# Kernel tuning notes

Hardware: AMD Instinct MI355X
Metric: run time of the kernel (lower is better)

## Reference

```python
import jax, jax.numpy as jnp
import numpy as np
from jax import lax

B, CIN, COUT, H, W = 16, 320, 320, 64, 64
R, NUM_LORAS, LORA_STRIDE, SCALE, K = 4, 50, 4, 1.0, 3


def setup_inputs() -> dict:
    key = jax.random.key(0)
    k1, k2, k3, k4, k5, k6 = jax.random.split(key, 6)
    x = jax.random.normal(k1, (B, CIN, H, W), dtype=jnp.float32)
    lora_id = jax.random.randint(k2, (B,), 0, NUM_LORAS * LORA_STRIDE, dtype=jnp.int64)
    conv_w = jax.random.normal(k3, (COUT, CIN, K, K), dtype=jnp.float32) * (1.0 / np.sqrt(CIN * K * K))
    conv_b = jax.random.normal(k4, (COUT,), dtype=jnp.float32) * 0.01
    # stacked LoRA banks: down [L, r, Cin, 3, 3], up [L, Cout, r] (1x1 conv squeezed)
    down_w = jax.random.normal(k5, (NUM_LORAS, R, CIN, K, K), dtype=jnp.float32) * (1.0 / R)
    up_w = jax.random.normal(k6, (NUM_LORAS, COUT, R), dtype=jnp.float32) * 0.02
    return {"x": x, "conv_w": conv_w, "conv_b": conv_b, "down_w": down_w, "up_w": up_w, "lora_id": lora_id}


def _conv3x3(x, w):
    # x: [N, C, H, W], w: [O, C, 3, 3], stride 1, padding 1
    return lax.conv_general_dilated(x, w, (1, 1), [(1, 1), (1, 1)],
                                    dimension_numbers=("NCHW", "OIHW", "NCHW"))


def reference(x, conv_w, conv_b, down_w, up_w, lora_id):
    idx = lora_id // LORA_STRIDE                      # [B]
    active = (idx >= 0).astype(x.dtype)               # [B] mask; negative -> base conv only
    safe = jnp.clip(idx, 0, NUM_LORAS - 1)
    # base conv on full batch (dropout is identity at inference)
    base = _conv3x3(x, conv_w) + conv_b[None, :, None, None]  # [B, Cout, H, W]
    # per-sample gathered down conv (3x3), vmapped over batch (MoE-style dispatch)
    wd = down_w[safe]                                 # [B, r, Cin, 3, 3]
    down = jax.vmap(lambda xi, wi: _conv3x3(xi[None], wi)[0])(x, wd)  # [B, r, H, W]
    # per-sample 1x1 up conv as einsum with gathered up weights
    up = jnp.einsum("brhw,bor->bohw", down, up_w[safe])  # [B, Cout, H, W]
    return base + SCALE * up * active[:, None, None, None]
```

## Files before the change

### kernel.cpp

```cpp
#include <hip/hip_runtime.h>

typedef unsigned short ushort_t;
typedef unsigned int   uint_t;
typedef __attribute__((ext_vector_type(8))) short  short8;
typedef __attribute__((ext_vector_type(4))) float  float4v;
typedef __attribute__((ext_vector_type(4))) uint_t uint4v;

#define B_    16
#define CIN_  320
#define COUT_ 320
#define NLORA 50
#define R_    4
#define NCH   10

#define XCHUNK (66*66*32)
#define WCHUNK (9*COUT_*32)
#define XPAD_ELEMS ((size_t)B_ * NCH * XCHUNK)
#define WEFF_OFF   (XPAD_ELEMS * 2)

__device__ __forceinline__ ushort_t bf16rne(float f) {
  uint_t u = __float_as_uint(f);
  u = (u + 0x7FFFu + ((u >> 16) & 1u)) >> 16;
  return (ushort_t)u;
}

__device__ __forceinline__ void gld16(const ushort_t* g, ushort_t* l) {
  __builtin_amdgcn_global_load_lds(
      (const __attribute__((address_space(1))) void*)g,
      (__attribute__((address_space(3))) void*)l,
      16, 0, 0);
}

__global__ __launch_bounds__(256)
void pad_convert(const float* __restrict__ x, ushort_t* __restrict__ x_pad) {
  __shared__ float t[64][65];
  const int cc  = blockIdx.x;
  const int h   = blockIdx.y;
  const int b   = blockIdx.z;
  const int tid = threadIdx.x;
  #pragma unroll
  for (int it = 0; it < 16; ++it) {
    int idx = it * 256 + tid;
    int cl = idx >> 6, wl = idx & 63;
    t[cl][wl] = x[(((size_t)(b * CIN_ + cc * 64 + cl)) * 64 + h) * 64 + wl];
  }
  __syncthreads();
  #pragma unroll
  for (int it = 0; it < 8; ++it) {
    int flat = (it * 256 + tid) * 2;
    int wl = flat >> 6, cl = flat & 63;
    uint_t u0 = bf16rne(t[cl][wl]);
    uint_t u1 = bf16rne(t[cl + 1][wl]);
    int chunk = cc * 2 + (cl >> 5);
    *(uint_t*)(x_pad + (((size_t)(b * NCH + chunk) * 66 + (h + 1)) * 66 + (wl + 1)) * 32
               + (cl & 31)) = u0 | (u1 << 16);
  }
  if (h == 0) {
    #pragma unroll
    for (int s = 0; s < 2; ++s) {
      ushort_t* base = x_pad + (size_t)(b * NCH + cc * 2 + s) * XCHUNK;
      for (int g = tid; g < 528; g += 256) {
        int r = (g >= 264) ? 1 : 0;
        int g2 = g - r * 264;
        int col = g2 >> 2, qg = g2 & 3;
        *(uint4v*)(base + ((size_t)(r * 65) * 66 + col) * 32 + qg * 8) = (uint4v)0u;
      }
      for (int g = tid; g < 512; g += 256) {
        int row = 1 + (g >> 3);
        int col = ((g >> 2) & 1) * 65;
        int qg  = g & 3;
        *(uint4v*)(base + ((size_t)row * 66 + col) * 32 + qg * 8) = (uint4v)0u;
      }
    }
  }
}

__global__ __launch_bounds__(320)
void merge_weights(const float* __restrict__ conv_w, const float* __restrict__ down_w,
                   const float* __restrict__ up_w,  const void* __restrict__ lora,
                   ushort_t* __restrict__ W_eff) {
  const int o = blockIdx.x;
  const int b = blockIdx.y;
  const int c = threadIdx.x;

  const int* p32 = (const int*)lora;
  bool odd0 = true;
  #pragma unroll
  for (int i = 1; i < 16; i += 2) odd0 = odd0 && (p32[i] == 0);
  long long raw = odd0 ? ((const long long*)lora)[b] : (long long)p32[b];
  long long idx = (raw >= 0) ? (raw >> 2) : -(((-raw) + 3) >> 2);
  float act = (idx >= 0) ? 1.0f : 0.0f;
  int l = (int)(idx < 0 ? 0 : (idx > (NLORA - 1) ? (NLORA - 1) : idx));

  float up[R_];
  #pragma unroll
  for (int r = 0; r < R_; ++r)
    up[r] = up_w[((size_t)l * COUT_ + o) * R_ + r] * act;

  const size_t wb = (size_t)(b * NCH + (c >> 5)) * 9;
  #pragma unroll
  for (int tap = 0; tap < 9; ++tap) {
    float v = conv_w[((size_t)o * CIN_ + c) * 9 + tap];
    #pragma unroll
    for (int r = 0; r < R_; ++r)
      v += up[r] * down_w[(((size_t)l * R_ + r) * CIN_ + c) * 9 + tap];
    W_eff[((wb + tap) * COUT_ + o) * 32 + (c & 31)] = bf16rne(v);
  }
}

#define XG    1360
#define XGP   1408
#define WG    1152
#define TOTG  2560
#define BUF_B (TOTG * 16)

__global__ __launch_bounds__(512, 4)
void conv_main(const ushort_t* __restrict__ x_pad, const ushort_t* __restrict__ W_eff,
               const float* __restrict__ conv_b, float* __restrict__ out) {
  __shared__ __align__(16) char smem[2 * BUF_B];

  const int tid = threadIdx.x;
  const int lin = blockIdx.x;
  const int wg  = (lin & 7) * 320 + (lin >> 3);
  const int b   = wg / 160;
  const int rem = wg - b * 160;
  const int o0  = (rem >> 4) * 32;
  const int hw  = rem & 15;
  const int h0  = (hw & 7) * 8;
  const int w0  = (hw >> 3) * 32;

  const int wv = tid >> 6;
  const int la = tid & 15;
  const int q  = (tid >> 4) & 3;

  const ushort_t* psrc[5];
  int step[5];
  #pragma unroll
  for (int r = 0; r < 5; ++r) {
    int g = r * 512 + tid;
    if (g < XGP) {
      int gx = (g < XG) ? g : (XG - 1);
      int qq = gx & 3, t = gx >> 2;
      int hh = t / 34, ww = t - hh * 34;
      psrc[r] = x_pad + (size_t)b * NCH * XCHUNK
              + (((h0 + hh) * 66 + (w0 + ww)) * 32 + qq * 8);
      step[r] = XCHUNK;
    } else {
      int gw = g - XGP;
      int qq = gw & 3, t2 = gw >> 2;
      int o = t2 & 31, tap = t2 >> 5;
      psrc[r] = W_eff + (size_t)b * NCH * WCHUNK
              + ((tap * COUT_ + o0 + o) * 32 + qq * 8);
      step[r] = WCHUNK;
    }
  }

  float4v acc[2][2];
  #pragma unroll
  for (int i = 0; i < 2; ++i)
    #pragma unroll
    for (int n = 0; n < 2; ++n) acc[i][n] = (float4v)0.0f;

  auto STAGE = [&](int sel) {
    ushort_t* bufb = (ushort_t*)(smem + sel * BUF_B);
    #pragma unroll
    for (int r = 0; r < 5; ++r) {
      gld16(psrc[r], bufb + (r * 512 + wv * 64) * 8);
      psrc[r] += step[r];
    }
  };

  STAGE(0);
  int cur = 0;
  for (int t = 0; t < NCH; ++t) {
    asm volatile("" ::: "memory");
    __builtin_amdgcn_s_barrier();
    asm volatile("" ::: "memory");
    if (t < NCH - 1) STAGE(cur ^ 1);
    __builtin_amdgcn_sched_barrier(0);
    if (t < NCH - 1) asm volatile("s_waitcnt vmcnt(5)" ::: "memory");
    else             asm volatile("s_waitcnt vmcnt(0)" ::: "memory");
    __builtin_amdgcn_sched_barrier(0);
    __builtin_amdgcn_s_barrier();
    asm volatile("" ::: "memory");

    const ushort_t* xb = (const ushort_t*)(smem + cur * BUF_B);
    const ushort_t* wb = xb + XGP * 8;
    #pragma unroll
    for (int tap = 0; tap < 9; ++tap) {
      const int kh = tap / 3, kw = tap - kh * 3;
      short8 bf0 = *(const short8*)(wb + ((tap * 32 +      la) * 4 + q) * 8);
      short8 bf1 = *(const short8*)(wb + ((tap * 32 + 16 + la) * 4 + q) * 8);
      const int hh = wv + kh;
      #pragma unroll
      for (int i = 0; i < 2; ++i) {
        short8 af = *(const short8*)(xb + ((hh * 34 + i * 16 + la + kw) * 4 + q) * 8);
        acc[i][0] = __builtin_amdgcn_mfma_f32_16x16x32_bf16(af, bf0, acc[i][0], 0, 0, 0);
        acc[i][1] = __builtin_amdgcn_mfma_f32_16x16x32_bf16(af, bf1, acc[i][1], 0, 0, 0);
      }
    }
    cur ^= 1;
  }

  __syncthreads();
  float* lc = (float*)smem;
  #pragma unroll
  for (int n = 0; n < 2; ++n) {
    const int n_loc = n * 16 + la;
    #pragma unroll
    for (int i = 0; i < 2; ++i)
      *(float4v*)(lc + n_loc * 260 + wv * 32 + i * 16 + q * 4) = acc[i][n];
  }
  __syncthreads();
  const size_t ob = ((size_t)(b * COUT_ + o0)) * 4096 + h0 * 64 + w0;
  for (int f = tid; f < 32 * 64; f += 512) {
    int n_loc = f >> 6;
    int m4 = (f & 63) * 4;
    int row = m4 >> 5, col = m4 & 31;
    float4v v = *(const float4v*)(lc + n_loc * 260 + m4);
    v += conv_b[o0 + n_loc];
    *(float4v*)(out + ob + (size_t)n_loc * 4096 + row * 64 + col) = v;
  }
}

extern "C" void kernel_launch(void* const* d_in, const int* in_sizes, int n_in,
                              void* d_out, int out_size, void* d_ws, size_t ws_size,
                              hipStream_t stream) {
  const float* x      = (const float*)d_in[0];
  const float* conv_w = (const float*)d_in[1];
  const float* conv_b = (const float*)d_in[2];
  const float* down_w = (const float*)d_in[3];
  const float* up_w   = (const float*)d_in[4];
  const void*  lora   = d_in[5];
  float* out = (float*)d_out;

  ushort_t* x_pad = (ushort_t*)d_ws;
  ushort_t* W_eff = (ushort_t*)((char*)d_ws + WEFF_OFF);

  pad_convert  <<<dim3(5, 64, 16), 256, 0, stream>>>(x, x_pad);
  merge_weights<<<dim3(320, 16),   320, 0, stream>>>(conv_w, down_w, up_w, lora, W_eff);
  conv_main    <<<dim3(2560),      512, 0, stream>>>(x_pad, W_eff, conv_b, out);
}
```

Baseline: 295.5 us.

## Swizzle LDS layout in conv main loop and vectorize prep kernels

```diff
diff --git a/kernel.cpp b/kernel.cpp
--- a/kernel.cpp
+++ b/kernel.cpp
@@ -5,6 +5,7 @@
 typedef __attribute__((ext_vector_type(8))) short  short8;
 typedef __attribute__((ext_vector_type(4))) float  float4v;
 typedef __attribute__((ext_vector_type(4))) uint_t uint4v;
+typedef __attribute__((ext_vector_type(2))) uint_t uint2v;
 
 #define B_    16
 #define CIN_  320
@@ -39,21 +40,26 @@
   const int b   = blockIdx.z;
   const int tid = threadIdx.x;
   #pragma unroll
-  for (int it = 0; it < 16; ++it) {
+  for (int it = 0; it < 4; ++it) {
     int idx = it * 256 + tid;
-    int cl = idx >> 6, wl = idx & 63;
-    t[cl][wl] = x[(((size_t)(b * CIN_ + cc * 64 + cl)) * 64 + h) * 64 + wl];
+    int cl = idx >> 4, w4 = (idx & 15) * 4;
+    float4v v = *(const float4v*)(x +
+        (((size_t)(b * CIN_ + cc * 64 + cl)) * 64 + h) * 64 + w4);
+    t[cl][w4] = v[0]; t[cl][w4 + 1] = v[1];
+    t[cl][w4 + 2] = v[2]; t[cl][w4 + 3] = v[3];
   }
   __syncthreads();
   #pragma unroll
-  for (int it = 0; it < 8; ++it) {
-    int flat = (it * 256 + tid) * 2;
-    int wl = flat >> 6, cl = flat & 63;
-    uint_t u0 = bf16rne(t[cl][wl]);
-    uint_t u1 = bf16rne(t[cl + 1][wl]);
+  for (int it = 0; it < 4; ++it) {
+    int j  = it * 256 + tid;
+    int cq = j & 15, wl = j >> 4;
+    int cl = cq * 4;
+    uint_t u0 = (uint_t)bf16rne(t[cl][wl])     | ((uint_t)bf16rne(t[cl + 1][wl]) << 16);
+    uint_t u1 = (uint_t)bf16rne(t[cl + 2][wl]) | ((uint_t)bf16rne(t[cl + 3][wl]) << 16);
     int chunk = cc * 2 + (cl >> 5);
-    *(uint_t*)(x_pad + (((size_t)(b * NCH + chunk) * 66 + (h + 1)) * 66 + (wl + 1)) * 32
-               + (cl & 31)) = u0 | (u1 << 16);
+    uint2v u; u[0] = u0; u[1] = u1;
+    *(uint2v*)(x_pad + (((size_t)(b * NCH + chunk) * 66 + (h + 1)) * 66 + (wl + 1)) * 32
+               + (cl & 31)) = u;
   }
   if (h == 0) {
     #pragma unroll
@@ -81,7 +87,7 @@
                    ushort_t* __restrict__ W_eff) {
   const int o = blockIdx.x;
   const int b = blockIdx.y;
-  const int c = threadIdx.x;
+  const int tid = threadIdx.x;
 
   const int* p32 = (const int*)lora;
   bool odd0 = true;
@@ -97,14 +103,17 @@
   for (int r = 0; r < R_; ++r)
     up[r] = up_w[((size_t)l * COUT_ + o) * R_ + r] * act;
 
-  const size_t wb = (size_t)(b * NCH + (c >> 5)) * 9;
-  #pragma unroll
-  for (int tap = 0; tap < 9; ++tap) {
-    float v = conv_w[((size_t)o * CIN_ + c) * 9 + tap];
-    #pragma unroll
-    for (int r = 0; r < R_; ++r)
-      v += up[r] * down_w[(((size_t)l * R_ + r) * CIN_ + c) * 9 + tap];
-    W_eff[((wb + tap) * COUT_ + o) * 32 + (c & 31)] = bf16rne(v);
+  const float* cw = conv_w + (size_t)o * (CIN_ * 9);
+  const float* dw = down_w + (size_t)l * (R_ * CIN_ * 9);
+  #pragma unroll
+  for (int it = 0; it < 9; ++it) {
+    int j = it * 320 + tid;
+    float v = cw[j] + up[0] * dw[j] + up[1] * dw[2880 + j]
+                    + up[2] * dw[5760 + j] + up[3] * dw[8640 + j];
+    int c   = j / 9;
+    int tap = j - c * 9;
+    W_eff[(((size_t)(b * NCH + (c >> 5)) * 9 + tap) * COUT_ + o) * 32 + (c & 31)]
+        = bf16rne(v);
   }
 }
 
@@ -142,15 +151,17 @@
       int gx = (g < XG) ? g : (XG - 1);
       int qq = gx & 3, t = gx >> 2;
       int hh = t / 34, ww = t - hh * 34;
+      int sq = qq ^ ((ww >> 1) & 3);
       psrc[r] = x_pad + (size_t)b * NCH * XCHUNK
-              + (((h0 + hh) * 66 + (w0 + ww)) * 32 + qq * 8);
+              + (((h0 + hh) * 66 + (w0 + ww)) * 32 + sq * 8);
       step[r] = XCHUNK;
     } else {
       int gw = g - XGP;
       int qq = gw & 3, t2 = gw >> 2;
       int o = t2 & 31, tap = t2 >> 5;
+      int sq = qq ^ ((o >> 1) & 3);
       psrc[r] = W_eff + (size_t)b * NCH * WCHUNK
-              + ((tap * COUT_ + o0 + o) * 32 + qq * 8);
+              + ((tap * COUT_ + o0 + o) * 32 + sq * 8);
       step[r] = WCHUNK;
     }
   }
@@ -189,12 +200,14 @@
     #pragma unroll
     for (int tap = 0; tap < 9; ++tap) {
       const int kh = tap / 3, kw = tap - kh * 3;
-      short8 bf0 = *(const short8*)(wb + ((tap * 32 +      la) * 4 + q) * 8);
-      short8 bf1 = *(const short8*)(wb + ((tap * 32 + 16 + la) * 4 + q) * 8);
+      const int ob0 = la, ob1 = 16 + la;
+      short8 bf0 = *(const short8*)(wb + ((tap * 32 + ob0) * 4 + (q ^ ((ob0 >> 1) & 3))) * 8);
+      short8 bf1 = *(const short8*)(wb + ((tap * 32 + ob1) * 4 + (q ^ ((ob1 >> 1) & 3))) * 8);
       const int hh = wv + kh;
       #pragma unroll
       for (int i = 0; i < 2; ++i) {
-        short8 af = *(const short8*)(xb + ((hh * 34 + i * 16 + la + kw) * 4 + q) * 8);
+        int ww = i * 16 + la + kw;
+        short8 af = *(const short8*)(xb + ((hh * 34 + ww) * 4 + (q ^ ((ww >> 1) & 3))) * 8);
         acc[i][0] = __builtin_amdgcn_mfma_f32_16x16x32_bf16(af, bf0, acc[i][0], 0, 0, 0);
         acc[i][1] = __builtin_amdgcn_mfma_f32_16x16x32_bf16(af, bf1, acc[i][1], 0, 0, 0);
       }
```

New measurement: 303.2 us. +2.6%, slower.
